# Kernel tuning notes

Measured on AMD Instinct MI355X. Metric: run time of the kernel, lower is better.

## Reference

```python
import jax, jax.numpy as jnp
import numpy as np

N_NODES = 50000


def _gcn_norm(edge_index, num_nodes):
    # Add self-loops (PyG GCNConv default) and compute symmetric norm.
    loops = jnp.arange(num_nodes, dtype=edge_index.dtype)
    src = jnp.concatenate([edge_index[0], loops])
    dst = jnp.concatenate([edge_index[1], loops])
    ones = jnp.ones(src.shape[0], dtype=jnp.float32)
    deg = jax.ops.segment_sum(ones, dst, num_segments=num_nodes)
    deg_inv_sqrt = jnp.where(deg > 0, jax.lax.rsqrt(jnp.maximum(deg, 1.0)), 0.0)
    norm = deg_inv_sqrt[src] * deg_inv_sqrt[dst]  # [E + N]
    return src, dst, norm


def _gcn_conv(x, src, dst, norm, W, b, num_nodes):
    xw = x @ W                               # [N, out]
    msg = xw[src] * norm[:, None]            # gather + scale  [E+N, out]
    out = jax.ops.segment_sum(msg, dst, num_segments=num_nodes)  # scatter-add
    return out + b


def setup_inputs() -> dict:
    key = jax.random.key(0)
    ks = jax.random.split(key, 10)
    d_in, d_h, d_out = 64, 64, 8
    n_edges = 800000
    x = jax.random.normal(ks[0], (N_NODES, d_in), dtype=jnp.float32)
    edge_index = jax.random.randint(ks[1], (2, n_edges), 0, N_NODES, dtype=jnp.int64)
    def w(k, fan_in, fan_out):
        return jax.random.normal(k, (fan_in, fan_out), dtype=jnp.float32) * (1.0 / np.sqrt(fan_in))
    return {
        "x": x,
        "edge_index": edge_index,
        "W0": w(ks[2], d_in, d_h), "b0": jnp.zeros((d_h,), jnp.float32),
        "W1": w(ks[3], d_h, d_h), "b1": jnp.zeros((d_h,), jnp.float32),
        "W2": w(ks[4], d_h, d_h), "b2": jnp.zeros((d_h,), jnp.float32),
        "linW": w(ks[5], d_h, d_out), "linb": jnp.zeros((d_out,), jnp.float32),
    }


def reference(x, edge_index, W0, b0, W1, b1, W2, b2, linW, linb):
    num_nodes = x.shape[0]
    src, dst, norm = _gcn_norm(edge_index, num_nodes)
    # 3 GCNConv layers, ReLU; dropout is identity at inference (training=False).
    for W, b in ((W0, b0), (W1, b1), (W2, b2)):
        x = jax.nn.relu(_gcn_conv(x, src, dst, norm, W, b, num_nodes))
    return x @ linW + linb
```

## Files before the change

kernel.cpp:

```cpp
#include <hip/hip_runtime.h>
#include <hip/hip_fp16.h>

#define TPB 256
#define CAP 16384
#define CAPSH 14
#define SC_BLOCKS 256

typedef __attribute__((ext_vector_type(8))) float f32x8;
typedef __attribute__((ext_vector_type(8))) unsigned short u16x8;
typedef __attribute__((ext_vector_type(4))) unsigned int u32x4;
typedef __attribute__((ext_vector_type(2))) _Float16 h16x2;


__device__ __forceinline__ int ld_idx(const void* p, long long i, int is64) {
    return is64 ? (int)((const long long*)p)[i] : ((const int*)p)[i];
}

__device__ __forceinline__ ushort4 f4_to_h4(float4 v) {
    ushort4 r;
    r.x = __half_as_ushort(__float2half_rn(v.x));
    r.y = __half_as_ushort(__float2half_rn(v.y));
    r.z = __half_as_ushort(__float2half_rn(v.z));
    r.w = __half_as_ushort(__float2half_rn(v.w));
    return r;
}

__global__ __launch_bounds__(TPB) void p3_scatter(const void* __restrict__ ei,
                                                  long long E,
                                                  int* __restrict__ gcur,
                                                  int* __restrict__ pairs) {
    __shared__ int cnt[TPB];
    __shared__ int cur2[TPB];
    __shared__ int s_is64;
    int t = threadIdx.x;
    if (t < 64) {
        const unsigned int* w = (const unsigned int*)ei;
        unsigned long long m = __ballot(w[2 * t + 1] != 0u);
        if (t == 0) s_is64 = (m == 0ull) ? 1 : 0;
    }
    cnt[t] = 0;
    __syncthreads();
    const int is64 = s_is64;
    long long chunk = (E + SC_BLOCKS - 1) / SC_BLOCKS;
    long long s0 = (long long)blockIdx.x * chunk;
    long long s1 = (s0 + chunk < E) ? s0 + chunk : E;

    for (long long e = s0 + t; e < s1; e += TPB) {
        int d = ld_idx(ei, E + e, is64);
        atomicAdd(&cnt[d >> 8], 1);
    }
    __syncthreads();
    if (cnt[t]) cur2[t] = (t << CAPSH) + atomicAdd(&gcur[t], cnt[t]);
    __syncthreads();
    for (long long e = s0 + t; e < s1; e += TPB) {
        int sv = ld_idx(ei, e, is64);
        int d  = ld_idx(ei, E + e, is64);
        int pos = atomicAdd(&cur2[d >> 8], 1);
        pairs[pos] = (sv << 8) | (d & 255);
    }
}

__global__ __launch_bounds__(TPB) void p4_fill(const int* __restrict__ pairs,
                                               const int* __restrict__ gcur,
                                               const float* __restrict__ x,
                                               int2* __restrict__ meta,
                                               int* __restrict__ csr,
                                               ushort4* __restrict__ z0, int N) {
    __shared__ int ldeg[TPB];
    __shared__ int ssc[TPB];
    __shared__ int cur[TPB];
    __shared__ float fdis[TPB];
    int t = threadIdx.x;
    int b = blockIdx.x;
    int base = b << CAPSH;
    int ecnt = gcur[b];
    ldeg[t] = 0;
    __syncthreads();
    for (int e = base + t; e < base + ecnt; e += TPB)
        atomicAdd(&ldeg[pairs[e] & 255], 1);
    __syncthreads();
    int dv = ldeg[t];
    int pv = (dv + 7) & ~7;
    ssc[t] = pv;
    __syncthreads();
    for (int off = 1; off < TPB; off <<= 1) {
        int u = 0;
        if (t >= off) u = ssc[t - off];
        __syncthreads();
        ssc[t] += u;
        __syncthreads();
    }
    int o = base + ssc[t] - pv;
    cur[t] = o;
    float dd = rsqrtf((float)(dv + 1));
    fdis[t] = dd;
    int node = (b << 8) + t;
    if (node < N)
        meta[node] = make_int2((o << 8) | (pv >> 3), __float_as_int(dd));
    __syncthreads();
    for (int e = base + t; e < base + ecnt; e += TPB) {
        int p = pairs[e];
        int pos = atomicAdd(&cur[p & 255], 1);
        csr[pos] = p >> 8;
    }
    for (int e = o + dv; e < o + pv; ++e) csr[e] = N;

    int ni = t >> 4, c = t & 15;
    for (int p = 0; p < 16; ++p) {
        int nd = (b << 8) + p * 16 + ni;
        if (nd < N) {
            float dvv = fdis[p * 16 + ni];
            float4 h = ((const float4*)x)[(size_t)nd * 16 + c];
            float4 r = {h.x * dvv, h.y * dvv, h.z * dvv, h.w * dvv};
            z0[(size_t)nd * 16 + c] = f4_to_h4(r);
        }
    }
    if (b == 0 && t < 16) z0[(size_t)N * 16 + t] = make_ushort4(0, 0, 0, 0);
}


#if __has_builtin(__builtin_amdgcn_fdot2) && __has_builtin(__builtin_amdgcn_perm)
#define GCN_DOT2 1
#else
#define GCN_DOT2 0
#endif

__device__ __forceinline__ void accum_row_pair(const u16x8& ra, const u16x8& rb,
                                               f32x8& acc) {
#if GCN_DOT2
    u32x4 a = __builtin_bit_cast(u32x4, ra);
    u32x4 b = __builtin_bit_cast(u32x4, rb);
    const h16x2 one = {(_Float16)1.0f, (_Float16)1.0f};
    #pragma unroll
    for (int j = 0; j < 4; ++j) {
        unsigned p0 = __builtin_amdgcn_perm(a[j], b[j], 0x05040100u);
        unsigned p1 = __builtin_amdgcn_perm(a[j], b[j], 0x07060302u);
        acc[2 * j]     = __builtin_amdgcn_fdot2(__builtin_bit_cast(h16x2, p0),
                                                one, acc[2 * j], false);
        acc[2 * j + 1] = __builtin_amdgcn_fdot2(__builtin_bit_cast(h16x2, p1),
                                                one, acc[2 * j + 1], false);
    }
#else
    #pragma unroll
    for (int i = 0; i < 8; ++i)
        acc[i] += __half2float(__ushort_as_half(ra[i])) +
                  __half2float(__ushort_as_half(rb[i]));
#endif
}

__device__ __forceinline__ void accum_batch(const u16x8 (&R)[8], f32x8& acc) {
    #pragma unroll
    for (int k = 0; k < 8; k += 2) accum_row_pair(R[k], R[k + 1], acc);
}

__device__ __forceinline__ void load_batch(const u16x8* __restrict__ z8,
                                           u16x8 (&R)[8], int idx, int c,
                                           int base) {
    #pragma unroll
    for (int k = 0; k < 8; ++k) {
        int s = __shfl(idx, base + k);
        R[k] = z8[(size_t)s * 8 + c];
    }
}

__device__ __forceinline__ f32x8 gather_rows(const u16x8* __restrict__ z8,
                                             const int* __restrict__ csr,
                                             int start, int nbatch, int c,
                                             f32x8 acc) {
    const int base = threadIdx.x & 56;
    if (nbatch <= 0) return acc;
    u16x8 A[8], B[8];
    int idx0 = csr[start + c];
    int idx_n = (nbatch > 1) ? csr[start + 8 + c] : 0;
    load_batch(z8, A, idx0, c, base);
    int bt = 0;
    for (;;) {
        int idx_f = (bt + 2 < nbatch) ? csr[start + (bt + 2) * 8 + c] : 0;
        if (bt + 1 < nbatch) load_batch(z8, B, idx_n, c, base);
        accum_batch(A, acc);
        if (++bt >= nbatch) break;
        int idx_f2 = (bt + 2 < nbatch) ? csr[start + (bt + 2) * 8 + c] : 0;
        if (bt + 1 < nbatch) load_batch(z8, A, idx_f, c, base);
        accum_batch(B, acc);
        if (++bt >= nbatch) break;
        idx_n = idx_f2;
    }
    return acc;
}

__device__ __forceinline__ f32x8 shfl_mm8(f32x8 s, const float4* Ws4, int c) {
    const int base = threadIdx.x & 56;
    f32x8 u = {0.f, 0.f, 0.f, 0.f, 0.f, 0.f, 0.f, 0.f};
    #pragma unroll
    for (int q = 0; q < 8; ++q) {
        #pragma unroll
        for (int r = 0; r < 8; ++r) {
            float hv = __shfl(s[r], base + q);
            float4 w0 = Ws4[(q * 8 + r) * 16 + 2 * c];
            float4 w1 = Ws4[(q * 8 + r) * 16 + 2 * c + 1];
            u[0] = fmaf(hv, w0.x, u[0]);
            u[1] = fmaf(hv, w0.y, u[1]);
            u[2] = fmaf(hv, w0.z, u[2]);
            u[3] = fmaf(hv, w0.w, u[3]);
            u[4] = fmaf(hv, w1.x, u[4]);
            u[5] = fmaf(hv, w1.y, u[5]);
            u[6] = fmaf(hv, w1.z, u[6]);
            u[7] = fmaf(hv, w1.w, u[7]);
        }
    }
    return u;
}

__device__ __forceinline__ u16x8 f8_to_h8(f32x8 v) {
    u16x8 r;
    #pragma unroll
    for (int i = 0; i < 8; ++i)
        r[i] = __half_as_ushort(__float2half_rn(v[i]));
    return r;
}

__global__ __launch_bounds__(TPB) void layer_mm(const u16x8* __restrict__ z,
                                                const int* __restrict__ csr,
                                                const int2* __restrict__ meta,
                                                const float* __restrict__ b,
                                                const float* __restrict__ W,
                                                u16x8* __restrict__ zout, int n) {
    __shared__ float Ws[64 * 64];
    int t = threadIdx.x;
    float4* Ws4 = (float4*)Ws;
    const float4* W4g = (const float4*)W;
    #pragma unroll
    for (int i = 0; i < 4; ++i) Ws4[t + i * TPB] = W4g[t + i * TPB];

    if (blockIdx.x == 0 && t < 8) {
        u16x8 zz = {0, 0, 0, 0, 0, 0, 0, 0};
        zout[(size_t)n * 8 + t] = zz;
    }
    __syncthreads();

    int wave = t >> 6, lane = t & 63;
    int g = lane >> 3, c = lane & 7;
    int node = blockIdx.x * 32 + wave * 8 + g;
    f32x8 s = {0.f, 0.f, 0.f, 0.f, 0.f, 0.f, 0.f, 0.f};
    float dv = 0.f;
    if (node < n) {
        int2 m = meta[node];
        int start = ((unsigned)m.x) >> 8;
        int nbatch = m.x & 255;
        dv = __int_as_float(m.y);
        u16x8 v = z[(size_t)node * 8 + c];
        #pragma unroll
        for (int i = 0; i < 8; ++i) s[i] = __half2float(__ushort_as_half(v[i]));
        s = gather_rows(z, csr, start, nbatch, c, s);
    }
    f32x8 u = shfl_mm8(s, Ws4, c);
    if (node < n) {
        float4 b0 = ((const float4*)b)[2 * c];
        float4 b1 = ((const float4*)b)[2 * c + 1];
        f32x8 r;
        r[0] = fmaxf(fmaf(dv, u[0], b0.x), 0.f) * dv;
        r[1] = fmaxf(fmaf(dv, u[1], b0.y), 0.f) * dv;
        r[2] = fmaxf(fmaf(dv, u[2], b0.z), 0.f) * dv;
        r[3] = fmaxf(fmaf(dv, u[3], b0.w), 0.f) * dv;
        r[4] = fmaxf(fmaf(dv, u[4], b1.x), 0.f) * dv;
        r[5] = fmaxf(fmaf(dv, u[5], b1.y), 0.f) * dv;
        r[6] = fmaxf(fmaf(dv, u[6], b1.z), 0.f) * dv;
        r[7] = fmaxf(fmaf(dv, u[7], b1.w), 0.f) * dv;
        zout[(size_t)node * 8 + c] = f8_to_h8(r);
    }
}

__global__ __launch_bounds__(TPB) void layer_final(const u16x8* __restrict__ z,
                                                   const int* __restrict__ csr,
                                                   const int2* __restrict__ meta,
                                                   const float* __restrict__ b,
                                                   const float* __restrict__ W,
                                                   const float* __restrict__ Wl,
                                                   const float* __restrict__ bl,
                                                   float* __restrict__ out, int n) {
    __shared__ float Ws[64 * 64];
    __shared__ float Wls[64 * 8];
    __shared__ float bls[8];
    int t = threadIdx.x;
    float4* Ws4 = (float4*)Ws;
    const float4* W4g = (const float4*)W;
    #pragma unroll
    for (int i = 0; i < 4; ++i) Ws4[t + i * TPB] = W4g[t + i * TPB];
    if (t < 128) ((float4*)Wls)[t] = ((const float4*)Wl)[t];
    if (t < 8) bls[t] = bl[t];
    __syncthreads();

    int wave = t >> 6, lane = t & 63;
    int g = lane >> 3, c = lane & 7;
    int node = blockIdx.x * 32 + wave * 8 + g;
    f32x8 s = {0.f, 0.f, 0.f, 0.f, 0.f, 0.f, 0.f, 0.f};
    float dv = 0.f;
    if (node < n) {
        int2 m = meta[node];
        int start = ((unsigned)m.x) >> 8;
        int nbatch = m.x & 255;
        dv = __int_as_float(m.y);
        u16x8 v = z[(size_t)node * 8 + c];
        #pragma unroll
        for (int i = 0; i < 8; ++i) s[i] = __half2float(__ushort_as_half(v[i]));
        s = gather_rows(z, csr, start, nbatch, c, s);
    }
    f32x8 u = shfl_mm8(s, Ws4, c);
    float4 b0 = ((const float4*)b)[2 * c];
    float4 b1 = ((const float4*)b)[2 * c + 1];
    f32x8 h;
    h[0] = fmaxf(fmaf(dv, u[0], b0.x), 0.f);
    h[1] = fmaxf(fmaf(dv, u[1], b0.y), 0.f);
    h[2] = fmaxf(fmaf(dv, u[2], b0.z), 0.f);
    h[3] = fmaxf(fmaf(dv, u[3], b0.w), 0.f);
    h[4] = fmaxf(fmaf(dv, u[4], b1.x), 0.f);
    h[5] = fmaxf(fmaf(dv, u[5], b1.y), 0.f);
    h[6] = fmaxf(fmaf(dv, u[6], b1.z), 0.f);
    h[7] = fmaxf(fmaf(dv, u[7], b1.w), 0.f);

    const int base = threadIdx.x & 56;
    float acc = bls[c];
    #pragma unroll
    for (int q = 0; q < 8; ++q) {
        #pragma unroll
        for (int r = 0; r < 8; ++r) {
            float hv = __shfl(h[r], base + q);
            acc = fmaf(hv, Wls[(q * 8 + r) * 8 + c], acc);
        }
    }
    if (node < n) out[(size_t)node * 8 + c] = acc;
}

extern "C" void kernel_launch(void* const* d_in, const int* in_sizes, int n_in,
                              void* d_out, int out_size, void* d_ws, size_t ws_size,
                              hipStream_t stream) {
    const float* x  = (const float*)d_in[0];
    const void*  ei = d_in[1];
    const float* W0 = (const float*)d_in[2];
    const float* b0 = (const float*)d_in[3];
    const float* W1 = (const float*)d_in[4];
    const float* b1 = (const float*)d_in[5];
    const float* W2 = (const float*)d_in[6];
    const float* b2 = (const float*)d_in[7];
    const float* Wl = (const float*)d_in[8];
    const float* bl = (const float*)d_in[9];

    const long long E = in_sizes[1] / 2;
    const int dh = in_sizes[3];
    const int din = in_sizes[2] / dh;
    const int N = in_sizes[0] / din;
    const int nb = (N + 255) >> 8;

    char* ws = (char*)d_ws;
    size_t off = 0;
    auto alloc = [&](size_t bytes) -> char* {
        char* r = ws + off;
        off += (bytes + 255) & ~(size_t)255;
        return r;
    };
    int*   gcur    = (int*)  alloc(1024);
    int2*  meta    = (int2*) alloc((size_t)N * 8);
    int*   pairs   = (int*)  alloc((size_t)nb * CAP * 4);
    int*   csr     = (int*)  alloc((size_t)nb * CAP * 4);
    u16x8* zbA     = (u16x8*)alloc((size_t)(N + 1) * 64 * 2);
    u16x8* zbB     = (u16x8*)alloc((size_t)(N + 1) * 64 * 2);

    hipMemsetAsync(gcur, 0, 256 * sizeof(int), stream);
    p3_scatter<<<SC_BLOCKS, TPB, 0, stream>>>(ei, E, gcur, pairs);
    p4_fill<<<nb, TPB, 0, stream>>>(pairs, gcur, x, meta, csr,
                                    (ushort4*)zbA, N);

    const int gL = (N + 31) / 32;
    layer_mm<<<gL, TPB, 0, stream>>>(zbA, csr, meta, b0, W0, zbB, N);
    layer_mm<<<gL, TPB, 0, stream>>>(zbB, csr, meta, b1, W1, zbA, N);
    layer_final<<<gL, TPB, 0, stream>>>(zbA, csr, meta, b2, W2, Wl, bl,
                                        (float*)d_out, N);
}
```

Measured before the change: 187.8 us.

## Fuse all phases into one persistent cooperative kernel with grid syncs

```diff
diff --git a/kernel.cpp b/kernel.cpp
--- a/kernel.cpp
+++ b/kernel.cpp
@@ -1,10 +1,12 @@
 #include <hip/hip_runtime.h>
 #include <hip/hip_fp16.h>
+#include <hip/hip_cooperative_groups.h>
+
+namespace cg = cooperative_groups;
 
 #define TPB 256
 #define CAP 16384
 #define CAPSH 14
-#define SC_BLOCKS 256
 
 typedef __attribute__((ext_vector_type(8))) float f32x8;
 typedef __attribute__((ext_vector_type(8))) unsigned short u16x8;
@@ -24,100 +26,6 @@
     r.w = __half_as_ushort(__float2half_rn(v.w));
     return r;
 }
-
-__global__ __launch_bounds__(TPB) void p3_scatter(const void* __restrict__ ei,
-                                                  long long E,
-                                                  int* __restrict__ gcur,
-                                                  int* __restrict__ pairs) {
-    __shared__ int cnt[TPB];
-    __shared__ int cur2[TPB];
-    __shared__ int s_is64;
-    int t = threadIdx.x;
-    if (t < 64) {
-        const unsigned int* w = (const unsigned int*)ei;
-        unsigned long long m = __ballot(w[2 * t + 1] != 0u);
-        if (t == 0) s_is64 = (m == 0ull) ? 1 : 0;
-    }
-    cnt[t] = 0;
-    __syncthreads();
-    const int is64 = s_is64;
-    long long chunk = (E + SC_BLOCKS - 1) / SC_BLOCKS;
-    long long s0 = (long long)blockIdx.x * chunk;
-    long long s1 = (s0 + chunk < E) ? s0 + chunk : E;
-
-    for (long long e = s0 + t; e < s1; e += TPB) {
-        int d = ld_idx(ei, E + e, is64);
-        atomicAdd(&cnt[d >> 8], 1);
-    }
-    __syncthreads();
-    if (cnt[t]) cur2[t] = (t << CAPSH) + atomicAdd(&gcur[t], cnt[t]);
-    __syncthreads();
-    for (long long e = s0 + t; e < s1; e += TPB) {
-        int sv = ld_idx(ei, e, is64);
-        int d  = ld_idx(ei, E + e, is64);
-        int pos = atomicAdd(&cur2[d >> 8], 1);
-        pairs[pos] = (sv << 8) | (d & 255);
-    }
-}
-
-__global__ __launch_bounds__(TPB) void p4_fill(const int* __restrict__ pairs,
-                                               const int* __restrict__ gcur,
-                                               const float* __restrict__ x,
-                                               int2* __restrict__ meta,
-                                               int* __restrict__ csr,
-                                               ushort4* __restrict__ z0, int N) {
-    __shared__ int ldeg[TPB];
-    __shared__ int ssc[TPB];
-    __shared__ int cur[TPB];
-    __shared__ float fdis[TPB];
-    int t = threadIdx.x;
-    int b = blockIdx.x;
-    int base = b << CAPSH;
-    int ecnt = gcur[b];
-    ldeg[t] = 0;
-    __syncthreads();
-    for (int e = base + t; e < base + ecnt; e += TPB)
-        atomicAdd(&ldeg[pairs[e] & 255], 1);
-    __syncthreads();
-    int dv = ldeg[t];
-    int pv = (dv + 7) & ~7;
-    ssc[t] = pv;
-    __syncthreads();
-    for (int off = 1; off < TPB; off <<= 1) {
-        int u = 0;
-        if (t >= off) u = ssc[t - off];
-        __syncthreads();
-        ssc[t] += u;
-        __syncthreads();
-    }
-    int o = base + ssc[t] - pv;
-    cur[t] = o;
-    float dd = rsqrtf((float)(dv + 1));
-    fdis[t] = dd;
-    int node = (b << 8) + t;
-    if (node < N)
-        meta[node] = make_int2((o << 8) | (pv >> 3), __float_as_int(dd));
-    __syncthreads();
-    for (int e = base + t; e < base + ecnt; e += TPB) {
-        int p = pairs[e];
-        int pos = atomicAdd(&cur[p & 255], 1);
-        csr[pos] = p >> 8;
-    }
-    for (int e = o + dv; e < o + pv; ++e) csr[e] = N;
-
-    int ni = t >> 4, c = t & 15;
-    for (int p = 0; p < 16; ++p) {
-        int nd = (b << 8) + p * 16 + ni;
-        if (nd < N) {
-            float dvv = fdis[p * 16 + ni];
-            float4 h = ((const float4*)x)[(size_t)nd * 16 + c];
-            float4 r = {h.x * dvv, h.y * dvv, h.z * dvv, h.w * dvv};
-            z0[(size_t)nd * 16 + c] = f4_to_h4(r);
-        }
-    }
-    if (b == 0 && t < 16) z0[(size_t)N * 16 + t] = make_ushort4(0, 0, 0, 0);
-}
-
 
 #if __has_builtin(__builtin_amdgcn_fdot2) && __has_builtin(__builtin_amdgcn_perm)
 #define GCN_DOT2 1
@@ -219,116 +127,233 @@
     return r;
 }
 
-__global__ __launch_bounds__(TPB) void layer_mm(const u16x8* __restrict__ z,
-                                                const int* __restrict__ csr,
-                                                const int2* __restrict__ meta,
-                                                const float* __restrict__ b,
-                                                const float* __restrict__ W,
-                                                u16x8* __restrict__ zout, int n) {
-    __shared__ float Ws[64 * 64];
-    int t = threadIdx.x;
-    float4* Ws4 = (float4*)Ws;
-    const float4* W4g = (const float4*)W;
-    #pragma unroll
-    for (int i = 0; i < 4; ++i) Ws4[t + i * TPB] = W4g[t + i * TPB];
-
-    if (blockIdx.x == 0 && t < 8) {
-        u16x8 zz = {0, 0, 0, 0, 0, 0, 0, 0};
-        zout[(size_t)n * 8 + t] = zz;
-    }
-    __syncthreads();
-
-    int wave = t >> 6, lane = t & 63;
-    int g = lane >> 3, c = lane & 7;
-    int node = blockIdx.x * 32 + wave * 8 + g;
-    f32x8 s = {0.f, 0.f, 0.f, 0.f, 0.f, 0.f, 0.f, 0.f};
-    float dv = 0.f;
-    if (node < n) {
-        int2 m = meta[node];
-        int start = ((unsigned)m.x) >> 8;
-        int nbatch = m.x & 255;
-        dv = __int_as_float(m.y);
-        u16x8 v = z[(size_t)node * 8 + c];
-        #pragma unroll
-        for (int i = 0; i < 8; ++i) s[i] = __half2float(__ushort_as_half(v[i]));
-        s = gather_rows(z, csr, start, nbatch, c, s);
-    }
-    f32x8 u = shfl_mm8(s, Ws4, c);
-    if (node < n) {
-        float4 b0 = ((const float4*)b)[2 * c];
-        float4 b1 = ((const float4*)b)[2 * c + 1];
-        f32x8 r;
-        r[0] = fmaxf(fmaf(dv, u[0], b0.x), 0.f) * dv;
-        r[1] = fmaxf(fmaf(dv, u[1], b0.y), 0.f) * dv;
-        r[2] = fmaxf(fmaf(dv, u[2], b0.z), 0.f) * dv;
-        r[3] = fmaxf(fmaf(dv, u[3], b0.w), 0.f) * dv;
-        r[4] = fmaxf(fmaf(dv, u[4], b1.x), 0.f) * dv;
-        r[5] = fmaxf(fmaf(dv, u[5], b1.y), 0.f) * dv;
-        r[6] = fmaxf(fmaf(dv, u[6], b1.z), 0.f) * dv;
-        r[7] = fmaxf(fmaf(dv, u[7], b1.w), 0.f) * dv;
-        zout[(size_t)node * 8 + c] = f8_to_h8(r);
-    }
-}
-
-__global__ __launch_bounds__(TPB) void layer_final(const u16x8* __restrict__ z,
-                                                   const int* __restrict__ csr,
-                                                   const int2* __restrict__ meta,
-                                                   const float* __restrict__ b,
-                                                   const float* __restrict__ W,
-                                                   const float* __restrict__ Wl,
-                                                   const float* __restrict__ bl,
-                                                   float* __restrict__ out, int n) {
+__global__ __launch_bounds__(TPB, 2) void fused_all(
+    const void* __restrict__ ei, long long E,
+    const float* __restrict__ x,
+    int* __restrict__ gcur, int* __restrict__ tick,
+    int* __restrict__ pairs, int2* __restrict__ meta, int* __restrict__ csr,
+    u16x8* __restrict__ zbA, u16x8* __restrict__ zbB,
+    const float* __restrict__ b0, const float* __restrict__ W0,
+    const float* __restrict__ b1, const float* __restrict__ W1,
+    const float* __restrict__ b2, const float* __restrict__ W2,
+    const float* __restrict__ Wl, const float* __restrict__ bl,
+    float* __restrict__ out, int N, int nbuck)
+{
+    cg::grid_group grid = cg::this_grid();
+    __shared__ int sA[TPB];
+    __shared__ int sB[TPB];
+    __shared__ float sdis[TPB];
+    __shared__ int s_is64;
     __shared__ float Ws[64 * 64];
     __shared__ float Wls[64 * 8];
     __shared__ float bls[8];
-    int t = threadIdx.x;
-    float4* Ws4 = (float4*)Ws;
-    const float4* W4g = (const float4*)W;
-    #pragma unroll
-    for (int i = 0; i < 4; ++i) Ws4[t + i * TPB] = W4g[t + i * TPB];
-    if (t < 128) ((float4*)Wls)[t] = ((const float4*)Wl)[t];
-    if (t < 8) bls[t] = bl[t];
-    __syncthreads();
-
-    int wave = t >> 6, lane = t & 63;
-    int g = lane >> 3, c = lane & 7;
-    int node = blockIdx.x * 32 + wave * 8 + g;
-    f32x8 s = {0.f, 0.f, 0.f, 0.f, 0.f, 0.f, 0.f, 0.f};
-    float dv = 0.f;
-    if (node < n) {
-        int2 m = meta[node];
-        int start = ((unsigned)m.x) >> 8;
-        int nbatch = m.x & 255;
-        dv = __int_as_float(m.y);
-        u16x8 v = z[(size_t)node * 8 + c];
+    const int t = threadIdx.x;
+    const int bid = blockIdx.x;
+    const int nblk = gridDim.x;
+
+    if (bid == 0) {
+        if (t < 256) gcur[t] = 0;
+        if (t < 8)   tick[t] = 0;
+    }
+    if (t < 64) {
+        const unsigned int* w = (const unsigned int*)ei;
+        unsigned long long m = __ballot(w[2 * t + 1] != 0u);
+        if (t == 0) s_is64 = (m == 0ull) ? 1 : 0;
+    }
+    __threadfence();
+    grid.sync();
+    const int is64 = s_is64;
+
+    {
+        long long chunk = (E + nblk - 1) / nblk;
+        long long c0 = (long long)bid * chunk;
+        long long c1 = (c0 + chunk < E) ? c0 + chunk : E;
+        sA[t] = 0;
+        __syncthreads();
+        for (long long e = c0 + t; e < c1; e += TPB) {
+            int d = ld_idx(ei, E + e, is64);
+            atomicAdd(&sA[d >> 8], 1);
+        }
+        __syncthreads();
+        if (sA[t]) sB[t] = (t << CAPSH) + atomicAdd(&gcur[t], sA[t]);
+        __syncthreads();
+        for (long long e = c0 + t; e < c1; e += TPB) {
+            int sv = ld_idx(ei, e, is64);
+            int d  = ld_idx(ei, E + e, is64);
+            int pos = atomicAdd(&sB[d >> 8], 1);
+            pairs[pos] = (sv << 8) | (d & 255);
+        }
+    }
+    __threadfence();
+    grid.sync();
+
+    for (int b = bid; b < nbuck; b += nblk) {
+        int base = b << CAPSH;
+        int ecnt = gcur[b];
+        sA[t] = 0;
+        __syncthreads();
+        for (int e = base + t; e < base + ecnt; e += TPB)
+            atomicAdd(&sA[pairs[e] & 255], 1);
+        __syncthreads();
+        int dvv = sA[t];
+        int pv = (dvv + 7) & ~7;
+        sB[t] = pv;
+        __syncthreads();
+        for (int off = 1; off < TPB; off <<= 1) {
+            int u = 0;
+            if (t >= off) u = sB[t - off];
+            __syncthreads();
+            sB[t] += u;
+            __syncthreads();
+        }
+        int o = base + sB[t] - pv;
+        sA[t] = o;
+        float dd = rsqrtf((float)(dvv + 1));
+        sdis[t] = dd;
+        int node = (b << 8) + t;
+        if (node < N)
+            meta[node] = make_int2((o << 8) | (pv >> 3), __float_as_int(dd));
+        __syncthreads();
+        for (int e = base + t; e < base + ecnt; e += TPB) {
+            int p = pairs[e];
+            int pos = atomicAdd(&sA[p & 255], 1);
+            csr[pos] = p >> 8;
+        }
+        for (int e = o + dvv; e < o + pv; ++e) csr[e] = N;
+
+        int ni = t >> 4, cc = t & 15;
+        ushort4* z0 = (ushort4*)zbA;
+        for (int p = 0; p < 16; ++p) {
+            int nd = (b << 8) + p * 16 + ni;
+            if (nd < N) {
+                float dsc = sdis[p * 16 + ni];
+                float4 h = ((const float4*)x)[(size_t)nd * 16 + cc];
+                float4 r = {h.x * dsc, h.y * dsc, h.z * dsc, h.w * dsc};
+                z0[(size_t)nd * 16 + cc] = f4_to_h4(r);
+            }
+        }
+        __syncthreads();
+    }
+    if (bid == 0 && t < 16)
+        ((ushort4*)zbA)[(size_t)N * 16 + t] = make_ushort4(0, 0, 0, 0);
+    __threadfence();
+    grid.sync();
+
+    const int lane = t & 63;
+    const int g = lane >> 3, c = lane & 7;
+    const int nwt = (N + 7) / 8;
+
+    #pragma unroll 1
+    for (int layer = 0; layer < 2; ++layer) {
+        const u16x8* z   = (layer == 0) ? zbA : zbB;
+        u16x8* zout      = (layer == 0) ? zbB : zbA;
+        const float* Wp  = (layer == 0) ? W0 : W1;
+        const float* bp  = (layer == 0) ? b0 : b1;
+        int* tk          = tick + layer;
+
+        float4* Ws4 = (float4*)Ws;
+        const float4* W4g = (const float4*)Wp;
         #pragma unroll
-        for (int i = 0; i < 8; ++i) s[i] = __half2float(__ushort_as_half(v[i]));
-        s = gather_rows(z, csr, start, nbatch, c, s);
-    }
-    f32x8 u = shfl_mm8(s, Ws4, c);
-    float4 b0 = ((const float4*)b)[2 * c];
-    float4 b1 = ((const float4*)b)[2 * c + 1];
-    f32x8 h;
-    h[0] = fmaxf(fmaf(dv, u[0], b0.x), 0.f);
-    h[1] = fmaxf(fmaf(dv, u[1], b0.y), 0.f);
-    h[2] = fmaxf(fmaf(dv, u[2], b0.z), 0.f);
-    h[3] = fmaxf(fmaf(dv, u[3], b0.w), 0.f);
-    h[4] = fmaxf(fmaf(dv, u[4], b1.x), 0.f);
-    h[5] = fmaxf(fmaf(dv, u[5], b1.y), 0.f);
-    h[6] = fmaxf(fmaf(dv, u[6], b1.z), 0.f);
-    h[7] = fmaxf(fmaf(dv, u[7], b1.w), 0.f);
-
-    const int base = threadIdx.x & 56;
-    float acc = bls[c];
-    #pragma unroll
-    for (int q = 0; q < 8; ++q) {
+        for (int i = 0; i < 4; ++i) Ws4[t + i * TPB] = W4g[t + i * TPB];
+        if (bid == 0 && t < 8) {
+            u16x8 zz = {0, 0, 0, 0, 0, 0, 0, 0};
+            zout[(size_t)N * 8 + t] = zz;
+        }
+        __syncthreads();
+
+        for (;;) {
+            int wt0 = 0;
+            if (lane == 0) wt0 = atomicAdd(tk, 1);
+            int wt = __shfl(wt0, 0);
+            if (wt >= nwt) break;
+            int node = wt * 8 + g;
+            f32x8 s = {0.f, 0.f, 0.f, 0.f, 0.f, 0.f, 0.f, 0.f};
+            float dv = 0.f;
+            if (node < N) {
+                int2 m = meta[node];
+                int start = ((unsigned)m.x) >> 8;
+                int nbatch = m.x & 255;
+                dv = __int_as_float(m.y);
+                u16x8 v = z[(size_t)node * 8 + c];
+                #pragma unroll
+                for (int i = 0; i < 8; ++i)
+                    s[i] = __half2float(__ushort_as_half(v[i]));
+                s = gather_rows(z, csr, start, nbatch, c, s);
+            }
+            f32x8 u = shfl_mm8(s, Ws4, c);
+            if (node < N) {
+                float4 bb0 = ((const float4*)bp)[2 * c];
+                float4 bb1 = ((const float4*)bp)[2 * c + 1];
+                f32x8 r;
+                r[0] = fmaxf(fmaf(dv, u[0], bb0.x), 0.f) * dv;
+                r[1] = fmaxf(fmaf(dv, u[1], bb0.y), 0.f) * dv;
+                r[2] = fmaxf(fmaf(dv, u[2], bb0.z), 0.f) * dv;
+                r[3] = fmaxf(fmaf(dv, u[3], bb0.w), 0.f) * dv;
+                r[4] = fmaxf(fmaf(dv, u[4], bb1.x), 0.f) * dv;
+                r[5] = fmaxf(fmaf(dv, u[5], bb1.y), 0.f) * dv;
+                r[6] = fmaxf(fmaf(dv, u[6], bb1.z), 0.f) * dv;
+                r[7] = fmaxf(fmaf(dv, u[7], bb1.w), 0.f) * dv;
+                zout[(size_t)node * 8 + c] = f8_to_h8(r);
+            }
+        }
+        __threadfence();
+        grid.sync();
+    }
+
+    {
+        float4* Ws4 = (float4*)Ws;
+        const float4* W4g = (const float4*)W2;
         #pragma unroll
-        for (int r = 0; r < 8; ++r) {
-            float hv = __shfl(h[r], base + q);
-            acc = fmaf(hv, Wls[(q * 8 + r) * 8 + c], acc);
-        }
-    }
-    if (node < n) out[(size_t)node * 8 + c] = acc;
+        for (int i = 0; i < 4; ++i) Ws4[t + i * TPB] = W4g[t + i * TPB];
+        if (t < 128) ((float4*)Wls)[t] = ((const float4*)Wl)[t];
+        if (t < 8) bls[t] = bl[t];
+        __syncthreads();
+
+        for (;;) {
+            int wt0 = 0;
+            if (lane == 0) wt0 = atomicAdd(tick + 2, 1);
+            int wt = __shfl(wt0, 0);
+            if (wt >= nwt) break;
+            int node = wt * 8 + g;
+            f32x8 s = {0.f, 0.f, 0.f, 0.f, 0.f, 0.f, 0.f, 0.f};
+            float dv = 0.f;
+            if (node < N) {
+                int2 m = meta[node];
+                int start = ((unsigned)m.x) >> 8;
+                int nbatch = m.x & 255;
+                dv = __int_as_float(m.y);
+                u16x8 v = zbA[(size_t)node * 8 + c];
+                #pragma unroll
+                for (int i = 0; i < 8; ++i)
+                    s[i] = __half2float(__ushort_as_half(v[i]));
+                s = gather_rows(zbA, csr, start, nbatch, c, s);
+            }
+            f32x8 u = shfl_mm8(s, Ws4, c);
+            float4 bb0 = ((const float4*)b2)[2 * c];
+            float4 bb1 = ((const float4*)b2)[2 * c + 1];
+            f32x8 h;
+            h[0] = fmaxf(fmaf(dv, u[0], bb0.x), 0.f);
+            h[1] = fmaxf(fmaf(dv, u[1], bb0.y), 0.f);
+            h[2] = fmaxf(fmaf(dv, u[2], bb0.z), 0.f);
+            h[3] = fmaxf(fmaf(dv, u[3], bb0.w), 0.f);
+            h[4] = fmaxf(fmaf(dv, u[4], bb1.x), 0.f);
+            h[5] = fmaxf(fmaf(dv, u[5], bb1.y), 0.f);
+            h[6] = fmaxf(fmaf(dv, u[6], bb1.z), 0.f);
+            h[7] = fmaxf(fmaf(dv, u[7], bb1.w), 0.f);
+
+            const int base = t & 56;
+            float acc = bls[c];
+            #pragma unroll
+            for (int qq = 0; qq < 8; ++qq) {
+                #pragma unroll
+                for (int rr = 0; rr < 8; ++rr) {
+                    float hv = __shfl(h[rr], base + qq);
+                    acc = fmaf(hv, Wls[(qq * 8 + rr) * 8 + c], acc);
+                }
+            }
+            if (node < N) out[(size_t)node * 8 + c] = acc;
+        }
+    }
 }
 
 extern "C" void kernel_launch(void* const* d_in, const int* in_sizes, int n_in,
@@ -345,11 +370,11 @@
     const float* Wl = (const float*)d_in[8];
     const float* bl = (const float*)d_in[9];
 
-    const long long E = in_sizes[1] / 2;
+    long long E = in_sizes[1] / 2;
     const int dh = in_sizes[3];
     const int din = in_sizes[2] / dh;
-    const int N = in_sizes[0] / din;
-    const int nb = (N + 255) >> 8;
+    int N = in_sizes[0] / din;
+    int nbuck = (N + 255) >> 8;
 
     char* ws = (char*)d_ws;
     size_t off = 0;
@@ -358,21 +383,34 @@
         off += (bytes + 255) & ~(size_t)255;
         return r;
     };
-    int*   gcur    = (int*)  alloc(1024);
-    int2*  meta    = (int2*) alloc((size_t)N * 8);
-    int*   pairs   = (int*)  alloc((size_t)nb * CAP * 4);
-    int*   csr     = (int*)  alloc((size_t)nb * CAP * 4);
-    u16x8* zbA     = (u16x8*)alloc((size_t)(N + 1) * 64 * 2);
-    u16x8* zbB     = (u16x8*)alloc((size_t)(N + 1) * 64 * 2);
-
-    hipMemsetAsync(gcur, 0, 256 * sizeof(int), stream);
-    p3_scatter<<<SC_BLOCKS, TPB, 0, stream>>>(ei, E, gcur, pairs);
-    p4_fill<<<nb, TPB, 0, stream>>>(pairs, gcur, x, meta, csr,
-                                    (ushort4*)zbA, N);
-
-    const int gL = (N + 31) / 32;
-    layer_mm<<<gL, TPB, 0, stream>>>(zbA, csr, meta, b0, W0, zbB, N);
-    layer_mm<<<gL, TPB, 0, stream>>>(zbB, csr, meta, b1, W1, zbA, N);
-    layer_final<<<gL, TPB, 0, stream>>>(zbA, csr, meta, b2, W2, Wl, bl,
-                                        (float*)d_out, N);
-}
+    int*   gcur  = (int*)  alloc(1024);
+    int*   tick  = (int*)  alloc(256);
+    int2*  meta  = (int2*) alloc((size_t)N * 8);
+    int*   pairs = (int*)  alloc((size_t)nbuck * CAP * 4);
+    int*   csr   = (int*)  alloc((size_t)nbuck * CAP * 4);
+    u16x8* zbA   = (u16x8*)alloc((size_t)(N + 1) * 64 * 2);
+    u16x8* zbB   = (u16x8*)alloc((size_t)(N + 1) * 64 * 2);
+    float* outp  = (float*)d_out;
+
+    static int gridBlocks = 0;
+    if (gridBlocks == 0) {
+        int perCU = 0, nCU = 0, dev = 0;
+        hipGetDevice(&dev);
+        hipOccupancyMaxActiveBlocksPerMultiprocessor(&perCU, fused_all, TPB, 0);
+        hipDeviceGetAttribute(&nCU, hipDeviceAttributeMultiprocessorCount, dev);
+        if (perCU < 1) perCU = 1;
+        if (nCU < 1) nCU = 256;
+        gridBlocks = perCU * nCU;
+        if (gridBlocks > 2048) gridBlocks = 2048;
+    }
+
+    void* args[] = {
+        (void*)&ei, (void*)&E, (void*)&x,
+        (void*)&gcur, (void*)&tick, (void*)&pairs, (void*)&meta, (void*)&csr,
+        (void*)&zbA, (void*)&zbB,
+        (void*)&b0, (void*)&W0, (void*)&b1, (void*)&W1, (void*)&b2, (void*)&W2,
+        (void*)&Wl, (void*)&bl, (void*)&outp, (void*)&N, (void*)&nbuck
+    };
+    hipLaunchCooperativeKernel((void*)fused_all, dim3(gridBlocks), dim3(TPB),
+                               args, 0, stream);
+}
```

Measured after the change: 642.1 us. 3.42x slower.

## Widen scatter grid, use 1024-thread fill blocks, and defer weight-load barrier

Applied to the files above, without the earlier changes.

```diff
diff --git a/kernel.cpp b/kernel.cpp
--- a/kernel.cpp
+++ b/kernel.cpp
@@ -2,9 +2,10 @@
 #include <hip/hip_fp16.h>
 
 #define TPB 256
+#define P4TPB 1024
 #define CAP 16384
 #define CAPSH 14
-#define SC_BLOCKS 256
+#define SC_BLOCKS 1024
 
 typedef __attribute__((ext_vector_type(8))) float f32x8;
 typedef __attribute__((ext_vector_type(8))) unsigned short u16x8;
@@ -29,8 +30,8 @@
                                                   long long E,
                                                   int* __restrict__ gcur,
                                                   int* __restrict__ pairs) {
-    __shared__ int cnt[TPB];
-    __shared__ int cur2[TPB];
+    __shared__ int cnt[256];
+    __shared__ int cur2[256];
     __shared__ int s_is64;
     int t = threadIdx.x;
     if (t < 64) {
@@ -60,56 +61,60 @@
     }
 }
 
-__global__ __launch_bounds__(TPB) void p4_fill(const int* __restrict__ pairs,
-                                               const int* __restrict__ gcur,
-                                               const float* __restrict__ x,
-                                               int2* __restrict__ meta,
-                                               int* __restrict__ csr,
-                                               ushort4* __restrict__ z0, int N) {
-    __shared__ int ldeg[TPB];
-    __shared__ int ssc[TPB];
-    __shared__ int cur[TPB];
-    __shared__ float fdis[TPB];
+__global__ __launch_bounds__(P4TPB) void p4_fill(const int* __restrict__ pairs,
+                                                 const int* __restrict__ gcur,
+                                                 const float* __restrict__ x,
+                                                 int2* __restrict__ meta,
+                                                 int* __restrict__ csr,
+                                                 ushort4* __restrict__ z0, int N) {
+    __shared__ int ldeg[256];
+    __shared__ int ssc[256];
+    __shared__ int cur[256];
+    __shared__ float fdis[256];
     int t = threadIdx.x;
     int b = blockIdx.x;
     int base = b << CAPSH;
     int ecnt = gcur[b];
-    ldeg[t] = 0;
-    __syncthreads();
-    for (int e = base + t; e < base + ecnt; e += TPB)
+    if (t < 256) ldeg[t] = 0;
+    __syncthreads();
+    for (int e = base + t; e < base + ecnt; e += P4TPB)
         atomicAdd(&ldeg[pairs[e] & 255], 1);
     __syncthreads();
-    int dv = ldeg[t];
+    int dv = (t < 256) ? ldeg[t] : 0;
     int pv = (dv + 7) & ~7;
-    ssc[t] = pv;
-    __syncthreads();
-    for (int off = 1; off < TPB; off <<= 1) {
+    if (t < 256) ssc[t] = pv;
+    __syncthreads();
+    for (int off = 1; off < 256; off <<= 1) {
         int u = 0;
-        if (t >= off) u = ssc[t - off];
+        if (t >= off && t < 256) u = ssc[t - off];
         __syncthreads();
-        ssc[t] += u;
+        if (t < 256) ssc[t] += u;
         __syncthreads();
     }
-    int o = base + ssc[t] - pv;
-    cur[t] = o;
-    float dd = rsqrtf((float)(dv + 1));
-    fdis[t] = dd;
-    int node = (b << 8) + t;
-    if (node < N)
-        meta[node] = make_int2((o << 8) | (pv >> 3), __float_as_int(dd));
-    __syncthreads();
-    for (int e = base + t; e < base + ecnt; e += TPB) {
+    int o = 0;
+    if (t < 256) {
+        o = base + ssc[t] - pv;
+        cur[t] = o;
+        float dd = rsqrtf((float)(dv + 1));
+        fdis[t] = dd;
+        int node = (b << 8) + t;
+        if (node < N)
+            meta[node] = make_int2((o << 8) | (pv >> 3), __float_as_int(dd));
+    }
+    __syncthreads();
+    for (int e = base + t; e < base + ecnt; e += P4TPB) {
         int p = pairs[e];
         int pos = atomicAdd(&cur[p & 255], 1);
         csr[pos] = p >> 8;
     }
-    for (int e = o + dv; e < o + pv; ++e) csr[e] = N;
+    if (t < 256)
+        for (int e = o + dv; e < o + pv; ++e) csr[e] = N;
 
     int ni = t >> 4, c = t & 15;
-    for (int p = 0; p < 16; ++p) {
-        int nd = (b << 8) + p * 16 + ni;
+    for (int p = 0; p < 4; ++p) {
+        int nd = (b << 8) + p * 64 + ni;
         if (nd < N) {
-            float dvv = fdis[p * 16 + ni];
+            float dvv = fdis[p * 64 + ni];
             float4 h = ((const float4*)x)[(size_t)nd * 16 + c];
             float4 r = {h.x * dvv, h.y * dvv, h.z * dvv, h.w * dvv};
             z0[(size_t)nd * 16 + c] = f4_to_h4(r);
@@ -236,7 +241,6 @@
         u16x8 zz = {0, 0, 0, 0, 0, 0, 0, 0};
         zout[(size_t)n * 8 + t] = zz;
     }
-    __syncthreads();
 
     int wave = t >> 6, lane = t & 63;
     int g = lane >> 3, c = lane & 7;
@@ -253,6 +257,7 @@
         for (int i = 0; i < 8; ++i) s[i] = __half2float(__ushort_as_half(v[i]));
         s = gather_rows(z, csr, start, nbatch, c, s);
     }
+    __syncthreads();
     f32x8 u = shfl_mm8(s, Ws4, c);
     if (node < n) {
         float4 b0 = ((const float4*)b)[2 * c];
@@ -288,7 +293,6 @@
     for (int i = 0; i < 4; ++i) Ws4[t + i * TPB] = W4g[t + i * TPB];
     if (t < 128) ((float4*)Wls)[t] = ((const float4*)Wl)[t];
     if (t < 8) bls[t] = bl[t];
-    __syncthreads();
 
     int wave = t >> 6, lane = t & 63;
     int g = lane >> 3, c = lane & 7;
@@ -305,6 +309,7 @@
         for (int i = 0; i < 8; ++i) s[i] = __half2float(__ushort_as_half(v[i]));
         s = gather_rows(z, csr, start, nbatch, c, s);
     }
+    __syncthreads();
     f32x8 u = shfl_mm8(s, Ws4, c);
     float4 b0 = ((const float4*)b)[2 * c];
     float4 b1 = ((const float4*)b)[2 * c + 1];
@@ -367,8 +372,8 @@
 
     hipMemsetAsync(gcur, 0, 256 * sizeof(int), stream);
     p3_scatter<<<SC_BLOCKS, TPB, 0, stream>>>(ei, E, gcur, pairs);
-    p4_fill<<<nb, TPB, 0, stream>>>(pairs, gcur, x, meta, csr,
-                                    (ushort4*)zbA, N);
+    p4_fill<<<nb, P4TPB, 0, stream>>>(pairs, gcur, x, meta, csr,
+                                      (ushort4*)zbA, N);
 
     const int gL = (N + 31) / 32;
     layer_mm<<<gL, TPB, 0, stream>>>(zbA, csr, meta, b0, W0, zbB, N);
```

Result: slower. 192.4 us (+2.5%).
